# Optimization experiments

Measured on AMD Instinct MI355X. Metric: run time of the kernel, lower is better.

## Reference

```python
import jax, jax.numpy as jnp
import numpy as np

B, S, D = 4, 2048, 1024


def setup_inputs() -> dict:
    key = jax.random.key(0)
    ks = jax.random.split(key, 4)
    scale = 1.0 / np.sqrt(D)
    x = jax.random.normal(ks[0], (B, S, D), dtype=jnp.float32)
    Wk = jax.random.normal(ks[1], (D, D), dtype=jnp.float32) * scale
    Wq = jax.random.normal(ks[2], (D, D), dtype=jnp.float32) * scale
    Wv = jax.random.normal(ks[3], (D, D), dtype=jnp.float32) * scale
    bk = jnp.zeros((D,), dtype=jnp.float32)
    bq = jnp.zeros((D,), dtype=jnp.float32)
    bv = jnp.zeros((D,), dtype=jnp.float32)
    return {"x": x, "Wk": Wk, "bk": bk, "Wq": Wq, "bq": bq,
            "Wv": Wv, "bv": bv, "dims": 2}


def correlated_weight(k, q, v, dims):
    # correlation between every query position and every key position,
    # scaled by sqrt(d) for numerical stability (standard correlation attn)
    d = q.shape[-1]
    scores = jnp.einsum("bqd,bkd->bqk", q, k) / jnp.sqrt(jnp.asarray(d, q.dtype))
    w = jax.nn.softmax(scores, axis=dims)          # [B, S, S]
    return jnp.einsum("bqk,bkd->bqd", w, v)        # [B, S, D]


def reference(x, Wk, bk, Wq, bq, Wv, bv, dims):
    # injected key/query/value funcs instantiated as Linear layers
    k = jnp.einsum("bsd,de->bse", x, Wk) + bk
    q = jnp.einsum("bsd,de->bse", x, Wq) + bq
    v = jnp.einsum("bsd,de->bse", x, Wv) + bv
    return correlated_weight(k, q, v, dims)
```

## Files before the change

### kernel.cpp

```cpp
#include <hip/hip_runtime.h>
#include <hip/hip_bf16.h>
#include <stdint.h>


typedef unsigned short u16;
typedef __bf16 bf16x8 __attribute__((ext_vector_type(8)));
typedef float  f32x4  __attribute__((ext_vector_type(4)));
typedef float  f32x16 __attribute__((ext_vector_type(16)));
typedef u16    u16x4  __attribute__((ext_vector_type(4)));
typedef u16    u16x8  __attribute__((ext_vector_type(8)));

__device__ __forceinline__ u16 f2bf(float f) {
  union { float f; uint32_t u; } v; v.f = f;
  uint32_t r = v.u + 0x7fffu + ((v.u >> 16) & 1u);
  return (u16)(r >> 16);
}
__device__ __forceinline__ float bf2f(u16 b) {
  union { uint32_t u; float f; } v; v.u = (uint32_t)b << 16; return v.f;
}

#define GLD_LDS16(gp, lp) __builtin_amdgcn_global_load_lds(                   \
    (const __attribute__((address_space(1))) void*)(gp),                      \
    (__attribute__((address_space(3))) void*)(lp), 16, 0, 0)


__global__ __launch_bounds__(256) void conv_x(const float* __restrict__ in,
                                              u16* __restrict__ out, int n) {
  int i = (blockIdx.x * 256 + threadIdx.x) * 4;
  if (i >= n) return;
  float4 v = *(const float4*)(in + i);
  u16x4 o; o.x = f2bf(v.x); o.y = f2bf(v.y); o.z = f2bf(v.z); o.w = f2bf(v.w);
  *(u16x4*)(out + i) = o;
}

__global__ __launch_bounds__(256) void trans_conv_w3(const float* __restrict__ Wq,
                                                     const float* __restrict__ Wk,
                                                     const float* __restrict__ Wv,
                                                     u16* __restrict__ Wt) {
  __shared__ float t[32][33];
  const float* W = blockIdx.z == 0 ? Wq : (blockIdx.z == 1 ? Wk : Wv);
  u16* dst = Wt + (size_t)blockIdx.z * 1024 * 1024;
  int e0 = blockIdx.x * 32, d0 = blockIdx.y * 32;
  #pragma unroll
  for (int i = 0; i < 4; ++i)
    t[threadIdx.y + i * 8][threadIdx.x] =
        W[(size_t)(d0 + threadIdx.y + i * 8) * 1024 + e0 + threadIdx.x];
  __syncthreads();
  #pragma unroll
  for (int i = 0; i < 4; ++i)
    dst[(size_t)(e0 + threadIdx.y + i * 8) * 1024 + d0 + threadIdx.x] =
        f2bf(t[threadIdx.x][threadIdx.y + i * 8]);
}

__global__ __launch_bounds__(256) void concat_bias(const float* __restrict__ bq,
                                                   const float* __restrict__ bk,
                                                   const float* __restrict__ bv,
                                                   float* __restrict__ bc) {
  int i = blockIdx.x * 256 + threadIdx.x;
  if (i >= 3072) return;
  bc[i] = (i < 1024) ? bq[i] : (i < 2048 ? bk[i - 1024] : bv[i - 2048]);
}

__global__ __launch_bounds__(256) void trans_v(const u16* __restrict__ qkv,
                                               u16* __restrict__ vT) {
  __shared__ u16 t[64][72];
  int b = blockIdx.z;
  int s0 = blockIdx.x * 64, e0 = blockIdx.y * 64;
  const u16* src = qkv + (size_t)b * 2048 * 3072 + 2048;
  u16* dst = vT + (size_t)b * 1024 * 2048;
  int tx = threadIdx.x & 7, ty = threadIdx.x >> 3;
  #pragma unroll
  for (int rr = 0; rr < 64; rr += 32)
    *(u16x8*)&t[ty + rr][tx * 8] =
        *(const u16x8*)(src + (size_t)(s0 + ty + rr) * 3072 + e0 + tx * 8);
  __syncthreads();
  #pragma unroll
  for (int rr = 0; rr < 64; rr += 32) {
    int er = ty + rr;
    u16x8 o;
    #pragma unroll
    for (int j = 0; j < 8; ++j) o[j] = t[tx * 8 + j][er];
    *(u16x8*)(dst + (size_t)(e0 + er) * 2048 + s0 + tx * 8) = o;
  }
}


#define FENCE8 asm volatile("" ::: "memory")
#define BARR8  do { FENCE8; __builtin_amdgcn_s_barrier(); FENCE8; } while (0)
#define WAITL8 asm volatile("s_waitcnt lgkmcnt(0)" ::: "memory")
#define VMW(N) asm volatile("s_waitcnt vmcnt(" #N ")" ::: "memory")

#define STAGE_A8(S, H, TT) do {                                               \
    GLD_LDS16(pA[H][0] + (TT) * 64,                                           \
              As + (S) * 16384 + ((H) * 64 + wv * 8) * 64);                   \
    GLD_LDS16(pA[H][1] + (TT) * 64,                                           \
              As + (S) * 16384 + ((H) * 64 + 128 + wv * 8) * 64);             \
  } while (0)

#define STAGE_B8(S, H, TT) do {                                               \
    GLD_LDS16(pB[H][0] + (TT) * 64,                                           \
              Bs + (S) * 16384 + ((H) * 32 + (wv >> 2) * 64 + (wv & 3) * 8) * 64); \
    GLD_LDS16(pB[H][1] + (TT) * 64,                                           \
              Bs + (S) * 16384 + ((H) * 32 + 128 + (wv >> 2) * 64 + (wv & 3) * 8) * 64); \
  } while (0)

#define RD_A8(S, MH) do {                                                     \
    _Pragma("unroll")                                                         \
    for (int mf = 0; mf < 4; ++mf) {                                          \
      const u16* p_ = As + (S) * 16384 + rdA + ((MH) * 64 + mf * 16) * 64;    \
      a[mf][0] = *(const bf16x8*)(p_ + pos0);                                 \
      a[mf][1] = *(const bf16x8*)(p_ + pos1);                                 \
    }                                                                         \
  } while (0)

#define RD_B8(S, NH) do {                                                     \
    _Pragma("unroll")                                                         \
    for (int nf = 0; nf < 2; ++nf) {                                          \
      const u16* p_ = Bs + (S) * 16384 + rdB + ((NH) * 32 + nf * 16) * 64;    \
      b[nf][0] = *(const bf16x8*)(p_ + pos0);                                 \
      b[nf][1] = *(const bf16x8*)(p_ + pos1);                                 \
    }                                                                         \
  } while (0)

#define MFMA_Q8(MH, NH) do {                                                  \
    _Pragma("unroll")                                                         \
    for (int ks = 0; ks < 2; ++ks)                                            \
      _Pragma("unroll")                                                       \
      for (int mf = 0; mf < 4; ++mf)                                          \
        _Pragma("unroll")                                                     \
        for (int nf = 0; nf < 2; ++nf)                                        \
          acc[(MH) * 4 + mf][(NH) * 2 + nf] =                                 \
              __builtin_amdgcn_mfma_f32_16x16x32_bf16(                        \
                  a[mf][ks], b[nf][ks], acc[(MH) * 4 + mf][(NH) * 2 + nf],    \
                  0, 0, 0);                                                   \
  } while (0)

#define GROUP8(S, T, EN1, EN2, WAITST) do {                                   \
    RD_A8(S, 0); RD_B8(S, 0);                                                 \
    if (EN1) STAGE_B8((S) ^ 1, 0, (T) + 1);                                   \
    BARR8; WAITL8;                                                            \
    __builtin_amdgcn_s_setprio(1); MFMA_Q8(0, 0);                             \
    __builtin_amdgcn_s_setprio(0); BARR8;                                     \
    RD_B8(S, 1);                                                              \
    if (EN2) STAGE_A8(S, 0, (T) + 2);                                         \
    BARR8; WAITL8;                                                            \
    __builtin_amdgcn_s_setprio(1); MFMA_Q8(0, 1);                             \
    __builtin_amdgcn_s_setprio(0); BARR8;                                     \
    RD_A8(S, 1);                                                              \
    if (EN2) STAGE_B8(S, 1, (T) + 2);                                         \
    BARR8; WAITL8;                                                            \
    __builtin_amdgcn_s_setprio(1); MFMA_Q8(1, 1);                             \
    __builtin_amdgcn_s_setprio(0); BARR8;                                     \
    RD_B8(S, 0);                                                              \
    if (EN2) STAGE_A8(S, 1, (T) + 2);                                         \
    BARR8; WAITL8;                                                            \
    __builtin_amdgcn_s_setprio(1); MFMA_Q8(1, 0);                             \
    __builtin_amdgcn_s_setprio(0); WAITST; BARR8;                             \
  } while (0)

template <int NT, bool OUT_BF16, bool BIAS>
__global__ __launch_bounds__(512)
void gemm8p(const u16* __restrict__ A, int lda, long long sA,
            const u16* __restrict__ B, int ldb, long long sB,
            void* __restrict__ C, int ldc, long long sC,
            const float* __restrict__ bias, float scale) {
  __shared__ __align__(16) u16 As[2 * 256 * 64];
  __shared__ __align__(16) u16 Bs[2 * 256 * 64];

  const int lane = threadIdx.x & 63;
  const int wv   = threadIdx.x >> 6;
  const int wm   = wv >> 2;
  const int wn   = wv & 3;
  const int l15  = lane & 15;
  const int hi4  = lane >> 4;
  const int rx7  = lane & 7;
  const int srow = lane >> 3;
  const int scem = ((lane & 7) ^ srow) * 8;

  const int nx = gridDim.x;
  const int flat = blockIdx.y * nx + blockIdx.x;
  const int nwg = nx * gridDim.y;
  const int cpx = nwg >> 3;
  const int swz = (flat & 7) * cpx + (flat >> 3);
  const int bx = swz % nx, by = swz / nx;

  const u16* Ab = A + (size_t)blockIdx.z * sA + (size_t)by * 256 * lda;
  const u16* Bb = B + (size_t)blockIdx.z * sB + (size_t)bx * 256 * ldb;

  const u16* pA[2][2];
  const u16* pB[2][2];
  #pragma unroll
  for (int h = 0; h < 2; ++h)
    #pragma unroll
    for (int r = 0; r < 2; ++r) {
      pA[h][r] = Ab + (size_t)(h * 64 + r * 128 + wv * 8 + srow) * lda + scem;
      pB[h][r] = Bb + (size_t)(h * 32 + r * 128 + (wv >> 2) * 64 +
                               (wv & 3) * 8 + srow) * ldb + scem;
    }

  const int rdA = (wm * 128 + l15) * 64;
  const int rdB = (wn * 64 + l15) * 64;
  const int pos0 = (hi4 ^ rx7) * 8;
  const int pos1 = ((4 + hi4) ^ rx7) * 8;

  f32x4 acc[8][4];
  #pragma unroll
  for (int i = 0; i < 8; ++i)
    #pragma unroll
    for (int j = 0; j < 4; ++j) acc[i][j] = (f32x4)0.0f;

  bf16x8 a[4][2], b[2][2];

  STAGE_A8(0, 0, 0); STAGE_B8(0, 1, 0); STAGE_A8(0, 1, 0); STAGE_B8(0, 0, 0);
  VMW(4);
  STAGE_A8(1, 0, 1); STAGE_B8(1, 1, 1); STAGE_A8(1, 1, 1);
  VMW(6);
  BARR8;

  #pragma unroll 1
  for (int i = 0; i < NT / 2 - 1; ++i) {
    const int t0 = 2 * i;
    GROUP8(0, t0,     1, 1, VMW(6));
    GROUP8(1, t0 + 1, 1, 1, VMW(6));
  }
  GROUP8(0, NT - 2, 1, 0, VMW(0));
  GROUP8(1, NT - 1, 0, 0, (void)0);

  const int m0 = by * 256 + wm * 128;
  const int n0 = bx * 256 + wn * 64;
  u16* Cb = (u16*)C + (size_t)blockIdx.z * sC;
  float* Cf = (float*)C + (size_t)blockIdx.z * sC;
  float bb[4];
  if (BIAS) {
    #pragma unroll
    for (int fn = 0; fn < 4; ++fn)
      bb[fn] = bias[n0 + (fn >> 1) * 32 + (fn & 1) * 16 + l15];
  }
  #pragma unroll
  for (int fm = 0; fm < 8; ++fm) {
    const int mb = m0 + (fm >> 2) * 64 + (fm & 3) * 16 + hi4 * 4;
    #pragma unroll
    for (int e = 0; e < 4; ++e) {
      const int m = mb + e;
      #pragma unroll
      for (int fn = 0; fn < 4; ++fn) {
        const int n = n0 + (fn >> 1) * 32 + (fn & 1) * 16 + l15;
        float v = acc[fm][fn][e] * scale;
        if (BIAS) v += bb[fn];
        if (OUT_BF16) Cb[(size_t)m * ldc + n] = f2bf(v);
        else          Cf[(size_t)m * ldc + n] = v;
      }
    }
  }
}

__global__ __launch_bounds__(512)
void gemm_bt8(const u16* __restrict__ A, int lda, long long sA,
              const u16* __restrict__ B, int ldb, long long sB,
              float* __restrict__ C, int ldc, long long sC,
              int K, float scale) {
  __shared__ u16 As[128 * 64];
  __shared__ u16 Bs[128 * 64];
  const int lane = threadIdx.x & 63;
  const int wv = threadIdx.x >> 6;

  const u16* Ab = A + (size_t)blockIdx.z * sA + (size_t)blockIdx.y * 128 * lda;
  const u16* Bb = B + (size_t)blockIdx.z * sB + (size_t)blockIdx.x * 128 * ldb;

  const int srow = lane >> 3;
  const int scol = ((lane & 7) ^ (lane >> 3)) * 8;
  const int r32 = lane & 31;
  const int half = lane >> 5;
  const int rx = lane & 7;
  const int wm = (wv >> 2) * 64;
  const int wn = (wv & 3) * 32;

  f32x16 acc[2];
  acc[0] = (f32x16)0.0f; acc[1] = (f32x16)0.0f;

  for (int k0 = 0; k0 < K; k0 += 64) {
    #pragma unroll
    for (int i = 0; i < 2; ++i) {
      int r = wv * 16 + i * 8;
      GLD_LDS16(Ab + (size_t)(r + srow) * lda + k0 + scol, As + r * 64);
      GLD_LDS16(Bb + (size_t)(r + srow) * ldb + k0 + scol, Bs + r * 64);
    }
    __syncthreads();

    bf16x8 af[2][4], bfr[4];
    #pragma unroll
    for (int t = 0; t < 4; ++t) {
      int pc = ((t * 2 + half) ^ rx) * 8;
      af[0][t] = *(const bf16x8*)(As + (wm + r32) * 64 + pc);
      af[1][t] = *(const bf16x8*)(As + (wm + 32 + r32) * 64 + pc);
      bfr[t]   = *(const bf16x8*)(Bs + (wn + r32) * 64 + pc);
    }
    #pragma unroll
    for (int i = 0; i < 2; ++i)
      #pragma unroll
      for (int t = 0; t < 4; ++t)
        acc[i] = __builtin_amdgcn_mfma_f32_32x32x16_bf16(
            af[i][t], bfr[t], acc[i], 0, 0, 0);
    __syncthreads();
  }

  const int ccol = blockIdx.x * 128 + wn + r32;
  const int crow0 = blockIdx.y * 128 + wm + 4 * half;
  float* Cf = C + (size_t)blockIdx.z * sC;
  #pragma unroll
  for (int i = 0; i < 2; ++i)
    #pragma unroll
    for (int e = 0; e < 16; ++e) {
      int m = crow0 + i * 32 + (e & 3) + 8 * (e >> 2);
      Cf[(size_t)m * ldc + ccol] = acc[i][e] * scale;
    }
}


__global__ __launch_bounds__(256) void softmax_rows(u16* __restrict__ P) {
  __shared__ float red[4];
  const int t = threadIdx.x;
  const int lane = t & 63, wv = t >> 6;
  u16* row = P + (size_t)blockIdx.x * 2048;
  u16x8 w = ((const u16x8*)row)[t];
  float v[8];
  #pragma unroll
  for (int j = 0; j < 8; ++j) v[j] = bf2f(w[j]);
  float m = v[0];
  #pragma unroll
  for (int j = 1; j < 8; ++j) m = fmaxf(m, v[j]);
  #pragma unroll
  for (int off = 32; off > 0; off >>= 1) m = fmaxf(m, __shfl_down(m, off));
  if (lane == 0) red[wv] = m;
  __syncthreads();
  m = fmaxf(fmaxf(red[0], red[1]), fmaxf(red[2], red[3]));
  __syncthreads();
  float e[8], s = 0.f;
  #pragma unroll
  for (int j = 0; j < 8; ++j) { e[j] = exp2f((v[j] - m) * 1.44269504f); s += e[j]; }
  #pragma unroll
  for (int off = 32; off > 0; off >>= 1) s += __shfl_down(s, off);
  if (lane == 0) red[wv] = s;
  __syncthreads();
  s = red[0] + red[1] + red[2] + red[3];
  float inv = 1.0f / s;
  u16x8 o;
  #pragma unroll
  for (int j = 0; j < 8; ++j) o[j] = f2bf(e[j] * inv);
  ((u16x8*)row)[t] = o;
}


extern "C" void kernel_launch(void* const* d_in, const int* in_sizes, int n_in,
                              void* d_out, int out_size, void* d_ws, size_t ws_size,
                              hipStream_t stream) {
  const float* x  = (const float*)d_in[0];
  const float* Wk = (const float*)d_in[1];
  const float* bk = (const float*)d_in[2];
  const float* Wq = (const float*)d_in[3];
  const float* bq = (const float*)d_in[4];
  const float* Wv = (const float*)d_in[5];
  const float* bv = (const float*)d_in[6];
  float* out = (float*)d_out;

  char* ws = (char*)d_ws;
  u16*   xb  = (u16*)(ws + 0);
  u16*   wt  = (u16*)(ws + 16777216);
  float* bc  = (float*)(ws + 23068672);
  u16*   qkv = (u16*)(ws + 23080960);
  u16*   vT  = (u16*)(ws + 73412608);
  u16*   P   = (u16*)(ws + 90189824);
  (void)in_sizes; (void)n_in; (void)out_size; (void)ws_size;

  conv_x<<<8192, 256, 0, stream>>>(x, xb, 8388608);
  trans_conv_w3<<<dim3(32, 32, 3), dim3(32, 8), 0, stream>>>(Wq, Wk, Wv, wt);
  concat_bias<<<12, 256, 0, stream>>>(bq, bk, bv, bc);

  gemm8p<16, true, true><<<dim3(12, 32, 1), 512, 0, stream>>>(
      xb, 1024, 0LL, wt, 1024, 0LL, (void*)qkv, 3072, 0LL, bc, 1.0f);

  trans_v<<<dim3(32, 16, 4), 256, 0, stream>>>(qkv, vT);

  gemm8p<16, true, false><<<dim3(8, 8, 4), 512, 0, stream>>>(
      qkv, 3072, 2048LL * 3072, qkv + 1024, 3072, 2048LL * 3072,
      (void*)P, 2048, 2048LL * 2048, nullptr, 0.03125f);

  softmax_rows<<<8192, 256, 0, stream>>>(P);

  gemm_bt8<<<dim3(8, 16, 4), 512, 0, stream>>>(
      P, 2048, 2048LL * 2048, vT, 2048, 1024LL * 2048,
      out, 1024, 2048LL * 1024, 2048, 1.0f);
}
```

Baseline: 273.8 us.

## Merge prep kernels and fuse V transpose into a new QKV GEMM epilogue

Folds the x conversion, weight transpose/convert and bias concat into one prep launch. The QKV projection moves from the pipelined 256x256 gemm8p to a simpler 128x128 single-buffered MFMA kernel. Blocks covering the V columns transpose their tile through LDS and write vT directly, which removes the separate trans_v pass and its round trip through qkv. The risk is that the new GEMM has no double buffering or prefetch, so it may run the large projection less efficiently than the tuned kernel it replaces.

```diff
diff --git a/kernel.cpp b/kernel.cpp
--- a/kernel.cpp
+++ b/kernel.cpp
@@ -24,63 +24,152 @@
     (__attribute__((address_space(3))) void*)(lp), 16, 0, 0)
 
 
-__global__ __launch_bounds__(256) void conv_x(const float* __restrict__ in,
-                                              u16* __restrict__ out, int n) {
-  int i = (blockIdx.x * 256 + threadIdx.x) * 4;
-  if (i >= n) return;
-  float4 v = *(const float4*)(in + i);
-  u16x4 o; o.x = f2bf(v.x); o.y = f2bf(v.y); o.z = f2bf(v.z); o.w = f2bf(v.w);
-  *(u16x4*)(out + i) = o;
-}
-
-__global__ __launch_bounds__(256) void trans_conv_w3(const float* __restrict__ Wq,
-                                                     const float* __restrict__ Wk,
-                                                     const float* __restrict__ Wv,
-                                                     u16* __restrict__ Wt) {
+__global__ __launch_bounds__(256)
+void prep_all(const float* __restrict__ x,
+              const float* __restrict__ Wq, const float* __restrict__ Wk,
+              const float* __restrict__ Wv,
+              const float* __restrict__ bq, const float* __restrict__ bk,
+              const float* __restrict__ bv,
+              u16* __restrict__ xb, u16* __restrict__ wt,
+              float* __restrict__ bc) {
   __shared__ float t[32][33];
-  const float* W = blockIdx.z == 0 ? Wq : (blockIdx.z == 1 ? Wk : Wv);
-  u16* dst = Wt + (size_t)blockIdx.z * 1024 * 1024;
-  int e0 = blockIdx.x * 32, d0 = blockIdx.y * 32;
-  #pragma unroll
-  for (int i = 0; i < 4; ++i)
-    t[threadIdx.y + i * 8][threadIdx.x] =
-        W[(size_t)(d0 + threadIdx.y + i * 8) * 1024 + e0 + threadIdx.x];
-  __syncthreads();
-  #pragma unroll
-  for (int i = 0; i < 4; ++i)
-    dst[(size_t)(e0 + threadIdx.y + i * 8) * 1024 + d0 + threadIdx.x] =
-        f2bf(t[threadIdx.x][threadIdx.y + i * 8]);
-}
-
-__global__ __launch_bounds__(256) void concat_bias(const float* __restrict__ bq,
-                                                   const float* __restrict__ bk,
-                                                   const float* __restrict__ bv,
-                                                   float* __restrict__ bc) {
-  int i = blockIdx.x * 256 + threadIdx.x;
-  if (i >= 3072) return;
-  bc[i] = (i < 1024) ? bq[i] : (i < 2048 ? bk[i - 1024] : bv[i - 2048]);
-}
-
-__global__ __launch_bounds__(256) void trans_v(const u16* __restrict__ qkv,
-                                               u16* __restrict__ vT) {
-  __shared__ u16 t[64][72];
-  int b = blockIdx.z;
-  int s0 = blockIdx.x * 64, e0 = blockIdx.y * 64;
-  const u16* src = qkv + (size_t)b * 2048 * 3072 + 2048;
-  u16* dst = vT + (size_t)b * 1024 * 2048;
-  int tx = threadIdx.x & 7, ty = threadIdx.x >> 3;
-  #pragma unroll
-  for (int rr = 0; rr < 64; rr += 32)
-    *(u16x8*)&t[ty + rr][tx * 8] =
-        *(const u16x8*)(src + (size_t)(s0 + ty + rr) * 3072 + e0 + tx * 8);
-  __syncthreads();
-  #pragma unroll
-  for (int rr = 0; rr < 64; rr += 32) {
-    int er = ty + rr;
+  const int bid = blockIdx.x;
+  if (bid < 4096) {
+    int i = (bid * 256 + threadIdx.x) * 8;
+    float4 v0 = *(const float4*)(x + i);
+    float4 v1 = *(const float4*)(x + i + 4);
     u16x8 o;
-    #pragma unroll
-    for (int j = 0; j < 8; ++j) o[j] = t[tx * 8 + j][er];
-    *(u16x8*)(dst + (size_t)(e0 + er) * 2048 + s0 + tx * 8) = o;
+    o[0] = f2bf(v0.x); o[1] = f2bf(v0.y); o[2] = f2bf(v0.z); o[3] = f2bf(v0.w);
+    o[4] = f2bf(v1.x); o[5] = f2bf(v1.y); o[6] = f2bf(v1.z); o[7] = f2bf(v1.w);
+    *(u16x8*)(xb + i) = o;
+  } else if (bid < 4096 + 3072) {
+    int b2 = bid - 4096;
+    int z = b2 >> 10, rem = b2 & 1023;
+    int e0 = (rem & 31) * 32, d0 = (rem >> 5) * 32;
+    const float* W = z == 0 ? Wq : (z == 1 ? Wk : Wv);
+    u16* dst = wt + (size_t)z * 1024 * 1024;
+    int tx = threadIdx.x & 31, ty = threadIdx.x >> 5;
+    #pragma unroll
+    for (int i = 0; i < 4; ++i)
+      t[ty + i * 8][tx] = W[(size_t)(d0 + ty + i * 8) * 1024 + e0 + tx];
+    __syncthreads();
+    #pragma unroll
+    for (int i = 0; i < 4; ++i)
+      dst[(size_t)(e0 + ty + i * 8) * 1024 + d0 + tx] =
+          f2bf(t[tx][ty + i * 8]);
+  } else {
+    int i = (bid - 7168) * 256 + threadIdx.x;
+    if (i < 3072)
+      bc[i] = (i < 1024) ? bq[i] : (i < 2048 ? bk[i - 1024] : bv[i - 2048]);
+  }
+}
+
+
+__global__ __launch_bounds__(256)
+void gemm_qkv(const u16* __restrict__ A, int lda,
+              const u16* __restrict__ B, int ldb,
+              u16* __restrict__ C, int ldc,
+              const float* __restrict__ bias, int K,
+              u16* __restrict__ vTp) {
+  __shared__ __align__(16) u16 smem[128 * 132];
+  u16* As = smem;
+  u16* Bs = smem + 8192;
+  const int lane = threadIdx.x & 63;
+  const int wv = threadIdx.x >> 6;
+
+  const u16* Ab = A + (size_t)blockIdx.y * 128 * lda;
+  const u16* Bb = B + (size_t)blockIdx.x * 128 * ldb;
+
+  const int srow = lane >> 3;
+  const int scol = ((lane & 7) ^ (lane >> 3)) * 8;
+  const int r32 = lane & 31;
+  const int half = lane >> 5;
+  const int rx = lane & 7;
+  const int wm = (wv >> 1) * 64;
+  const int wn = (wv & 1) * 64;
+
+  f32x16 acc[2][2];
+  #pragma unroll
+  for (int i = 0; i < 2; ++i)
+    #pragma unroll
+    for (int j = 0; j < 2; ++j) acc[i][j] = (f32x16)0.0f;
+
+  for (int k0 = 0; k0 < K; k0 += 64) {
+    #pragma unroll
+    for (int i = 0; i < 4; ++i) {
+      int r = wv * 32 + i * 8;
+      GLD_LDS16(Ab + (size_t)(r + srow) * lda + k0 + scol, As + r * 64);
+      GLD_LDS16(Bb + (size_t)(r + srow) * ldb + k0 + scol, Bs + r * 64);
+    }
+    __syncthreads();
+
+    bf16x8 af[2][4], bfr[2][4];
+    #pragma unroll
+    for (int i = 0; i < 2; ++i)
+      #pragma unroll
+      for (int t = 0; t < 4; ++t) {
+        int pc = ((t * 2 + half) ^ rx) * 8;
+        af[i][t]  = *(const bf16x8*)(As + (wm + i * 32 + r32) * 64 + pc);
+        bfr[i][t] = *(const bf16x8*)(Bs + (wn + i * 32 + r32) * 64 + pc);
+      }
+    #pragma unroll
+    for (int i = 0; i < 2; ++i)
+      #pragma unroll
+      for (int j = 0; j < 2; ++j)
+        #pragma unroll
+        for (int t = 0; t < 4; ++t)
+          acc[i][j] = __builtin_amdgcn_mfma_f32_32x32x16_bf16(
+              af[i][t], bfr[j][t], acc[i][j], 0, 0, 0);
+    __syncthreads();
+  }
+
+  if (blockIdx.x < 16) {
+    const int ccol0 = blockIdx.x * 128 + wn + r32;
+    const int crow0 = blockIdx.y * 128 + wm + 4 * half;
+    #pragma unroll
+    for (int i = 0; i < 2; ++i) {
+      #pragma unroll
+      for (int e = 0; e < 16; ++e) {
+        int m = crow0 + i * 32 + (e & 3) + 8 * (e >> 2);
+        #pragma unroll
+        for (int j = 0; j < 2; ++j) {
+          int n = ccol0 + j * 32;
+          C[(size_t)m * ldc + n] = f2bf(acc[i][j][e] + bias[n]);
+        }
+      }
+    }
+  } else {
+    u16 (*t)[132] = (u16(*)[132])smem;
+    #pragma unroll
+    for (int i = 0; i < 2; ++i) {
+      #pragma unroll
+      for (int j = 0; j < 2; ++j) {
+        const int nl = wn + j * 32 + r32;
+        const float bv = bias[blockIdx.x * 128 + nl];
+        #pragma unroll
+        for (int eg = 0; eg < 4; ++eg) {
+          const int mb = wm + i * 32 + 4 * half + 8 * eg;
+          u16x4 o;
+          #pragma unroll
+          for (int q = 0; q < 4; ++q) o[q] = f2bf(acc[i][j][eg * 4 + q] + bv);
+          *(u16x4*)&t[nl][mb] = o;
+        }
+      }
+    }
+    __syncthreads();
+    const int tid = threadIdx.x;
+    const int bb = blockIdx.y >> 4;
+    const int s0 = (blockIdx.y & 15) * 128 + (tid & 15) * 8;
+    const int e_base = (blockIdx.x - 16) * 128;
+    u16* dstb = vTp + (size_t)bb * 1024 * 2048;
+    #pragma unroll
+    for (int p = 0; p < 8; ++p) {
+      const int el = (tid >> 4) + p * 16;
+      u16x8 o;
+      #pragma unroll
+      for (int q = 0; q < 8; ++q) o[q] = t[el][(tid & 15) * 8 + q];
+      *(u16x8*)(dstb + (size_t)(e_base + el) * 2048 + s0) = o;
+    }
   }
 }
 
@@ -158,12 +247,11 @@
     __builtin_amdgcn_s_setprio(0); WAITST; BARR8;                             \
   } while (0)
 
-template <int NT, bool OUT_BF16, bool BIAS>
+template <int NT>
 __global__ __launch_bounds__(512)
 void gemm8p(const u16* __restrict__ A, int lda, long long sA,
             const u16* __restrict__ B, int ldb, long long sB,
-            void* __restrict__ C, int ldc, long long sC,
-            const float* __restrict__ bias, float scale) {
+            u16* __restrict__ C, int ldc, long long sC, float scale) {
   __shared__ __align__(16) u16 As[2 * 256 * 64];
   __shared__ __align__(16) u16 Bs[2 * 256 * 64];
 
@@ -228,14 +316,7 @@
 
   const int m0 = by * 256 + wm * 128;
   const int n0 = bx * 256 + wn * 64;
-  u16* Cb = (u16*)C + (size_t)blockIdx.z * sC;
-  float* Cf = (float*)C + (size_t)blockIdx.z * sC;
-  float bb[4];
-  if (BIAS) {
-    #pragma unroll
-    for (int fn = 0; fn < 4; ++fn)
-      bb[fn] = bias[n0 + (fn >> 1) * 32 + (fn & 1) * 16 + l15];
-  }
+  u16* Cb = C + (size_t)blockIdx.z * sC;
   #pragma unroll
   for (int fm = 0; fm < 8; ++fm) {
     const int mb = m0 + (fm >> 2) * 64 + (fm & 3) * 16 + hi4 * 4;
@@ -245,10 +326,7 @@
       #pragma unroll
       for (int fn = 0; fn < 4; ++fn) {
         const int n = n0 + (fn >> 1) * 32 + (fn & 1) * 16 + l15;
-        float v = acc[fm][fn][e] * scale;
-        if (BIAS) v += bb[fn];
-        if (OUT_BF16) Cb[(size_t)m * ldc + n] = f2bf(v);
-        else          Cf[(size_t)m * ldc + n] = v;
+        Cb[(size_t)m * ldc + n] = f2bf(acc[fm][fn][e] * scale);
       }
     }
   }
@@ -372,18 +450,14 @@
   u16*   P   = (u16*)(ws + 90189824);
   (void)in_sizes; (void)n_in; (void)out_size; (void)ws_size;
 
-  conv_x<<<8192, 256, 0, stream>>>(x, xb, 8388608);
-  trans_conv_w3<<<dim3(32, 32, 3), dim3(32, 8), 0, stream>>>(Wq, Wk, Wv, wt);
-  concat_bias<<<12, 256, 0, stream>>>(bq, bk, bv, bc);
-
-  gemm8p<16, true, true><<<dim3(12, 32, 1), 512, 0, stream>>>(
-      xb, 1024, 0LL, wt, 1024, 0LL, (void*)qkv, 3072, 0LL, bc, 1.0f);
-
-  trans_v<<<dim3(32, 16, 4), 256, 0, stream>>>(qkv, vT);
-
-  gemm8p<16, true, false><<<dim3(8, 8, 4), 512, 0, stream>>>(
+  prep_all<<<7180, 256, 0, stream>>>(x, Wq, Wk, Wv, bq, bk, bv, xb, wt, bc);
+
+  gemm_qkv<<<dim3(24, 64, 1), 256, 0, stream>>>(
+      xb, 1024, wt, 1024, qkv, 3072, bc, 1024, vT);
+
+  gemm8p<16><<<dim3(8, 8, 4), 512, 0, stream>>>(
       qkv, 3072, 2048LL * 3072, qkv + 1024, 3072, 2048LL * 3072,
-      (void*)P, 2048, 2048LL * 2048, nullptr, 0.03125f);
+      P, 2048, 2048LL * 2048, 0.03125f);
 
   softmax_rows<<<8192, 256, 0, stream>>>(P);
 
```

Measured after the change: 262.8 us. 4.0% less time.
